# Kernel tuning notes

Hardware: AMD Instinct MI355X
Metric: run time of the kernel (lower is better)

Reference implementation:

```python
import jax, jax.numpy as jnp
import numpy as np

BLOCK = 256


def setup_inputs() -> dict:
    key = jax.random.key(0)
    ks = jax.random.split(key, 6)
    b, n, hid = 2, 4096, 2048
    h, d = 16, 128
    x = jax.random.normal(ks[0], (b, n, hid), dtype=jnp.float32)
    slope_rate = jax.random.uniform(ks[1], (h, 1, 1), dtype=jnp.float32)
    Wqkv = jax.random.normal(ks[2], (3 * h * d, hid), dtype=jnp.float32) * 0.02
    Wg = jax.random.normal(ks[3], (h * d, hid), dtype=jnp.float32) * 0.02
    norm_w = jnp.ones((h * d,), dtype=jnp.float32)
    Wo = jax.random.normal(ks[4], (hid, h * d), dtype=jnp.float32) * 0.02
    return {"x": x, "slope_rate": slope_rate, "Wqkv": Wqkv, "Wg": Wg, "norm_w": norm_w, "Wo": Wo}


def reference(x, slope_rate, Wqkv, Wg, norm_w, Wo):
    b, n, hid = x.shape
    h = slope_rate.shape[0]
    d = Wqkv.shape[0] // (3 * h)
    nb = n // BLOCK

    qkv = jax.nn.silu(x @ Wqkv.T).reshape(b, n, h, 3 * d)
    q, k, v = jnp.split(qkv, 3, axis=-1)           # each (b, n, h, d)
    # -> (b, h, n, d)
    q = q.transpose(0, 2, 1, 3)
    k = k.transpose(0, 2, 1, 3)
    v = v.transpose(0, 2, 1, 3)

    s = slope_rate.astype(jnp.float32)             # (h, 1, 1)
    arr = jnp.arange(1, BLOCK + 1, dtype=jnp.float32)
    q_decay = jnp.exp(-s * arr[:, None])           # (h, BLOCK, 1)
    k_decay = jnp.exp(-s * (BLOCK - arr[:, None])) # (h, BLOCK, 1)
    idx = arr[:, None] - arr[None, :]              # (BLOCK, BLOCK)
    diag_decay = jnp.where(idx >= 0, jnp.exp(-s * idx), 0.0)  # (h, BLOCK, BLOCK)
    block_decay = jnp.exp(-s * BLOCK)              # (h, 1, 1)

    # chunk into blocks: (nb, b, h, BLOCK, d)
    def chunk(t):
        return t.reshape(b, h, nb, BLOCK, d).transpose(2, 0, 1, 3, 4)
    qc, kc, vc = chunk(q), chunk(k), chunk(v)

    def step(kv, qkv_blk):
        qi, ki, vi = qkv_blk
        # inter-block: decayed query against running kv state
        out_nd = jnp.einsum('bhmd,bhde->bhme', qi * q_decay, kv)
        # intra-block: decay-masked quadratic attention
        qk = jnp.einsum('bhmd,bhnd->bhmn', qi, ki) * diag_decay
        out_d = jnp.einsum('bhmn,bhne->bhme', qk, vi)
        kv_new = block_decay * kv + jnp.einsum('bhmd,bhme->bhde', ki * k_decay, vi)
        return kv_new, out_nd + out_d

    kv0 = jnp.zeros((b, h, d, d), dtype=jnp.float32)
    _, out_blocks = jax.lax.scan(step, kv0, (qc, kc, vc))  # (nb, b, h, BLOCK, d)

    out = out_blocks.transpose(1, 2, 0, 3, 4).reshape(b, h, n, d)
    out = out.transpose(0, 2, 1, 3).reshape(b, n, h * d)  # b n (h d)

    # RMSNorm
    eps = jnp.finfo(jnp.float32).eps
    rms = jax.lax.rsqrt(jnp.mean(out * out, axis=-1, keepdims=True) + eps)
    out = out * rms * norm_w

    gate = jax.nn.sigmoid(x @ Wg.T)
    return (gate * out) @ Wo.T
```

## Files before the change

### kernel.cpp

```cpp
#include <hip/hip_runtime.h>
#include <stdint.h>

typedef __attribute__((ext_vector_type(8))) short short8;
typedef __attribute__((ext_vector_type(4))) float f32x4;

#define DEV static __device__ __forceinline__

DEV float b2f(unsigned short u) {
  unsigned x = ((unsigned)u) << 16;
  return __builtin_bit_cast(float, x);
}
DEV unsigned short f2b(float f) {
  unsigned x = __builtin_bit_cast(unsigned, f);
  return (unsigned short)((x + 0x7fffu + ((x >> 16) & 1u)) >> 16);
}
DEV void gload16(const unsigned short* g, unsigned short* l) {
  __builtin_amdgcn_global_load_lds((const __attribute__((address_space(1))) void*)g,
                                   (__attribute__((address_space(3))) void*)l, 16, 0, 0);
}
#define MFMA(a, b, c) __builtin_amdgcn_mfma_f32_16x16x32_bf16(a, b, c, 0, 0, 0)

__global__ void k_f2b(const float* __restrict__ in, unsigned short* __restrict__ out, long n) {
  long i = ((long)blockIdx.x * blockDim.x + threadIdx.x) * 4;
  long stride = (long)gridDim.x * blockDim.x * 4;
  for (; i < n; i += stride) {
    float4 f = *(const float4*)(in + i);
    ushort4 o;
    o.x = f2b(f.x); o.y = f2b(f.y); o.z = f2b(f.z); o.w = f2b(f.w);
    *(ushort4*)(out + i) = o;
  }
}

template <int MODE>
__global__ __launch_bounds__(256, 2) void k_gemm(
    const unsigned short* __restrict__ A, const unsigned short* __restrict__ B0,
    const unsigned short* __restrict__ B1, int K, int NB0,
    unsigned short* __restrict__ o_q, unsigned short* __restrict__ o_k,
    unsigned short* __restrict__ o_v, unsigned short* __restrict__ o_g,
    float* __restrict__ o_f) {
  __shared__ unsigned short a_sh[128 * 32];
  __shared__ unsigned short b_sh[128 * 32];
  int tid = threadIdx.x;
  int w = tid >> 6, lane = tid & 63;
  int brow = blockIdx.x * 128, bcol = blockIdx.y * 128;
  const unsigned short* Bt = (MODE == 1 || bcol < NB0) ? (B0 + (size_t)bcol * K)
                                                       : (B1 + (size_t)(bcol - NB0) * K);
  int wrow = (w >> 1) * 64, wcol = (w & 1) * 64;
  f32x4 acc[4][4];
#pragma unroll
  for (int m = 0; m < 4; m++)
#pragma unroll
    for (int n = 0; n < 4; n++) acc[m][n] = (f32x4)0.f;

  int srow = lane >> 2;
  int scol = (lane & 3) * 8;
  int nk = K >> 5;
  for (int it = 0; it < nk; ++it) {
    int kt = it << 5;
    __syncthreads();
#pragma unroll
    for (int c = 0; c < 2; ++c) {
      int hseg = w * 2 + c;
      int row = hseg * 16 + srow;
      gload16(A + (size_t)(brow + row) * K + kt + scol, a_sh + hseg * 512 + lane * 8);
      gload16(Bt + (size_t)row * K + kt + scol, b_sh + hseg * 512 + lane * 8);
    }
    __syncthreads();
    int ko = (lane >> 4) * 8;
    short8 af[4], bfr[4];
#pragma unroll
    for (int m = 0; m < 4; m++)
      af[m] = *(const short8*)(a_sh + (wrow + m * 16 + (lane & 15)) * 32 + ko);
#pragma unroll
    for (int n = 0; n < 4; n++)
      bfr[n] = *(const short8*)(b_sh + (wcol + n * 16 + (lane & 15)) * 32 + ko);
#pragma unroll
    for (int m = 0; m < 4; m++)
#pragma unroll
      for (int n = 0; n < 4; n++) acc[m][n] = MFMA(af[m], bfr[n], acc[m][n]);
  }
#pragma unroll
  for (int m = 0; m < 4; m++) {
#pragma unroll
    for (int r = 0; r < 4; r++) {
      int row = brow + wrow + m * 16 + (lane >> 4) * 4 + r;
#pragma unroll
      for (int n = 0; n < 4; n++) {
        int col = bcol + wcol + n * 16 + (lane & 15);
        float v = acc[m][n][r];
        if (MODE == 0) {
          if (col < 6144) {
            float sv = v / (1.f + __expf(-v));
            int h = col / 384, dd = col - h * 384;
            int b = row >> 12, t = row & 4095;
            size_t base = ((size_t)(b * 16 + h) * 4096 + t) * 128;
            if (dd < 128) o_q[base + dd] = f2b(sv);
            else if (dd < 256) o_k[base + dd - 128] = f2b(sv);
            else o_v[base + dd - 256] = f2b(sv);
          } else {
            float gv = 1.f / (1.f + __expf(-v));
            o_g[(size_t)row * 2048 + (col - 6144)] = f2b(gv);
          }
        } else {
          o_f[(size_t)row * ((size_t)gridDim.y * 128) + col] = v;
        }
      }
    }
  }
}

__global__ __launch_bounds__(256) void k_kvblk(const unsigned short* __restrict__ kk,
                                               const unsigned short* __restrict__ vv,
                                               const float* __restrict__ slope,
                                               unsigned short* __restrict__ kvT) {
  int gid = blockIdx.x;
  int bh = gid >> 4, blk = gid & 15;
  float s = slope[bh & 15];
  __shared__ unsigned short kT[128][72];
  __shared__ unsigned short vT[128][72];
  int tid = threadIdx.x, w = tid >> 6, lane = tid & 63;
  int wrow = (w >> 1) * 64, wcol = (w & 1) * 64;
  f32x4 acc[4][4];
#pragma unroll
  for (int m = 0; m < 4; m++)
#pragma unroll
    for (int n = 0; n < 4; n++) acc[m][n] = (f32x4)0.f;
  const unsigned short* kb = kk + ((size_t)bh * 4096 + blk * 256) * 128;
  const unsigned short* vb = vv + ((size_t)bh * 4096 + blk * 256) * 128;
  int tt = tid & 63, c0 = (tid >> 6) * 32;
  for (int tc = 0; tc < 4; ++tc) {
    __syncthreads();
    int tg = tc * 64 + tt;
    float kd = __expf(-s * (float)(255 - tg));
#pragma unroll
    for (int g = 0; g < 4; ++g) {
      int c = c0 + g * 8;
      short8 k8 = *(const short8*)(kb + (size_t)tg * 128 + c);
      short8 v8 = *(const short8*)(vb + (size_t)tg * 128 + c);
#pragma unroll
      for (int j = 0; j < 8; ++j) {
        kT[c + j][tt] = f2b(b2f((unsigned short)k8[j]) * kd);
        vT[c + j][tt] = (unsigned short)v8[j];
      }
    }
    __syncthreads();
#pragma unroll
    for (int kx = 0; kx < 64; kx += 32) {
      int ko = kx + (lane >> 4) * 8;
      short8 af[4], bfr[4];
#pragma unroll
      for (int m = 0; m < 4; m++) af[m] = *(const short8*)&vT[wrow + m * 16 + (lane & 15)][ko];
#pragma unroll
      for (int n = 0; n < 4; n++) bfr[n] = *(const short8*)&kT[wcol + n * 16 + (lane & 15)][ko];
#pragma unroll
      for (int m = 0; m < 4; m++)
#pragma unroll
        for (int n = 0; n < 4; n++) acc[m][n] = MFMA(af[m], bfr[n], acc[m][n]);
    }
  }
  unsigned short* op = kvT + (size_t)gid * 16384;
#pragma unroll
  for (int m = 0; m < 4; m++)
#pragma unroll
    for (int r = 0; r < 4; r++) {
      int e = wrow + m * 16 + (lane >> 4) * 4 + r;
#pragma unroll
      for (int n = 0; n < 4; n++) {
        int d = wcol + n * 16 + (lane & 15);
        op[e * 128 + d] = f2b(acc[m][n][r]);
      }
    }
}

__global__ void k_scan(unsigned short* kvT, const float* __restrict__ slope) {
  int gid = blockIdx.x;
  int bh = gid >> 6;
  int eo = (gid & 63) * 256 + threadIdx.x;
  float s = slope[bh & 15];
  float bd = __expf(-s * 256.f);
  float st = 0.f;
  size_t base = (size_t)bh * 16 * 16384 + eo;
#pragma unroll
  for (int i = 0; i < 16; ++i) {
    unsigned short c = kvT[base + (size_t)i * 16384];
    kvT[base + (size_t)i * 16384] = f2b(st);
    st = bd * st + b2f(c);
  }
}

__global__ __launch_bounds__(256) void k_attn(const unsigned short* __restrict__ q,
                                              const unsigned short* __restrict__ kk,
                                              const unsigned short* __restrict__ vv,
                                              const unsigned short* __restrict__ kvT,
                                              const float* __restrict__ slope,
                                              unsigned short* __restrict__ attn) {
  int gid = blockIdx.x;
  int hf = gid & 1, blk = (gid >> 1) & 15, bh = gid >> 5;
  float s = slope[bh & 15];
  __shared__ unsigned short k_sh[64][136];
  __shared__ unsigned short vT_sh[128][72];
  __shared__ unsigned short s_sh[4][32][72];
  int tid = threadIdx.x, w = tid >> 6, lane = tid & 63;
  int mm0 = hf * 128 + w * 32;
  const unsigned short* qb = q + ((size_t)bh * 4096 + blk * 256) * 128;
  const unsigned short* kvb = kvT + (size_t)(bh * 16 + blk) * 16384;
  f32x4 acc[2][8];
#pragma unroll
  for (int m = 0; m < 2; m++)
#pragma unroll
    for (int n = 0; n < 8; n++) acc[m][n] = (f32x4)0.f;
#pragma unroll
  for (int kx = 0; kx < 128; kx += 32) {
    int ko = kx + (lane >> 4) * 8;
    short8 af[2], bfr[8];
#pragma unroll
    for (int mi = 0; mi < 2; mi++)
      af[mi] = *(const short8*)(qb + (size_t)(mm0 + mi * 16 + (lane & 15)) * 128 + ko);
#pragma unroll
    for (int ni = 0; ni < 8; ni++)
      bfr[ni] = *(const short8*)(kvb + (size_t)(ni * 16 + (lane & 15)) * 128 + ko);
#pragma unroll
    for (int mi = 0; mi < 2; mi++)
#pragma unroll
      for (int ni = 0; ni < 8; ni++) acc[mi][ni] = MFMA(af[mi], bfr[ni], acc[mi][ni]);
  }
#pragma unroll
  for (int mi = 0; mi < 2; mi++)
#pragma unroll
    for (int r = 0; r < 4; r++) {
      float qd = __expf(-s * (float)(mm0 + mi * 16 + (lane >> 4) * 4 + r + 1));
#pragma unroll
      for (int ni = 0; ni < 8; ni++) acc[mi][ni][r] *= qd;
    }
  int nchunk = 2 * (hf + 1);
  for (int tc = 0; tc < nchunk; ++tc) {
    __syncthreads();
    {
      int t2 = tid >> 2, c = (tid & 3) * 32;
      const unsigned short* kp = kk + ((size_t)bh * 4096 + blk * 256 + tc * 64 + t2) * 128 + c;
#pragma unroll
      for (int g = 0; g < 4; ++g) *(short8*)&k_sh[t2][c + g * 8] = *(const short8*)(kp + g * 8);
    }
    {
      int t2 = tid & 63, e0 = (tid >> 6) * 32;
      const unsigned short* vp = vv + ((size_t)bh * 4096 + blk * 256 + tc * 64 + t2) * 128 + e0;
#pragma unroll
      for (int g = 0; g < 4; ++g) {
        short8 v8 = *(const short8*)(vp + g * 8);
#pragma unroll
        for (int j = 0; j < 8; ++j) vT_sh[e0 + g * 8 + j][t2] = (unsigned short)v8[j];
      }
    }
    __syncthreads();
    if (tc * 64 <= mm0 + 31) {
      f32x4 sa[2][4];
#pragma unroll
      for (int m = 0; m < 2; m++)
#pragma unroll
        for (int n = 0; n < 4; n++) sa[m][n] = (f32x4)0.f;
#pragma unroll
      for (int kx = 0; kx < 128; kx += 32) {
        int ko = kx + (lane >> 4) * 8;
        short8 af[2], bfr[4];
#pragma unroll
        for (int mi = 0; mi < 2; mi++)
          af[mi] = *(const short8*)(qb + (size_t)(mm0 + mi * 16 + (lane & 15)) * 128 + ko);
#pragma unroll
        for (int ni = 0; ni < 4; ni++) bfr[ni] = *(const short8*)&k_sh[ni * 16 + (lane & 15)][ko];
#pragma unroll
        for (int mi = 0; mi < 2; mi++)
#pragma unroll
          for (int ni = 0; ni < 4; ni++) sa[mi][ni] = MFMA(af[mi], bfr[ni], sa[mi][ni]);
      }
#pragma unroll
      for (int mi = 0; mi < 2; mi++)
#pragma unroll
        for (int ni = 0; ni < 4; ni++)
#pragma unroll
          for (int r = 0; r < 4; r++) {
            int mm = mm0 + mi * 16 + (lane >> 4) * 4 + r;
            int ttg = tc * 64 + ni * 16 + (lane & 15);
            int diff = mm - ttg;
            float val = (diff >= 0) ? sa[mi][ni][r] * __expf(-s * (float)diff) : 0.f;
            s_sh[w][mi * 16 + (lane >> 4) * 4 + r][ni * 16 + (lane & 15)] = f2b(val);
          }
#pragma unroll
      for (int k2 = 0; k2 < 64; k2 += 32) {
        int ko2 = k2 + (lane >> 4) * 8;
        short8 a2[2];
#pragma unroll
        for (int mi = 0; mi < 2; mi++)
          a2[mi] = *(const short8*)&s_sh[w][mi * 16 + (lane & 15)][ko2];
#pragma unroll
        for (int ni = 0; ni < 8; ni++) {
          short8 b2 = *(const short8*)&vT_sh[ni * 16 + (lane & 15)][ko2];
#pragma unroll
          for (int mi = 0; mi < 2; mi++) acc[mi][ni] = MFMA(a2[mi], b2, acc[mi][ni]);
        }
      }
    }
  }
  int b = bh >> 4, h = bh & 15;
#pragma unroll
  for (int mi = 0; mi < 2; mi++)
#pragma unroll
    for (int r = 0; r < 4; r++) {
      int mm = mm0 + mi * 16 + (lane >> 4) * 4 + r;
      size_t rowp = ((size_t)b * 4096 + blk * 256 + mm) * 2048 + h * 128;
#pragma unroll
      for (int ni = 0; ni < 8; ni++) attn[rowp + ni * 16 + (lane & 15)] = f2b(acc[mi][ni][r]);
    }
}

__global__ __launch_bounds__(256) void k_norm(const unsigned short* __restrict__ attn,
                                              const unsigned short* __restrict__ gate,
                                              const float* __restrict__ nw,
                                              unsigned short* __restrict__ y) {
  int row = blockIdx.x;
  int tid = threadIdx.x, w = tid >> 6, lane = tid & 63;
  const unsigned short* ap = attn + (size_t)row * 2048 + tid * 8;
  const unsigned short* gp = gate + (size_t)row * 2048 + tid * 8;
  short8 a8 = *(const short8*)ap;
  float vals[8];
  float ss = 0.f;
#pragma unroll
  for (int j = 0; j < 8; ++j) {
    vals[j] = b2f((unsigned short)a8[j]);
    ss += vals[j] * vals[j];
  }
#pragma unroll
  for (int off = 32; off > 0; off >>= 1) ss += __shfl_down(ss, off, 64);
  __shared__ float red[4];
  if (lane == 0) red[w] = ss;
  __syncthreads();
  float tot = red[0] + red[1] + red[2] + red[3];
  float rms = rsqrtf(tot * (1.f / 2048.f) + 1.1920929e-07f);
  short8 g8 = *(const short8*)gp;
  short8 o;
#pragma unroll
  for (int j = 0; j < 8; ++j)
    o[j] = (short)f2b(vals[j] * rms * nw[tid * 8 + j] * b2f((unsigned short)g8[j]));
  *(short8*)(y + (size_t)row * 2048 + tid * 8) = o;
}

extern "C" void kernel_launch(void* const* d_in, const int* in_sizes, int n_in, void* d_out,
                              int out_size, void* d_ws, size_t ws_size, hipStream_t stream) {
  const float* x = (const float*)d_in[0];
  const float* slope = (const float*)d_in[1];
  const float* Wqkv = (const float*)d_in[2];
  const float* Wg = (const float*)d_in[3];
  const float* nw = (const float*)d_in[4];
  const float* Wo = (const float*)d_in[5];
  float* out = (float*)d_out;

  unsigned short* q = (unsigned short*)d_ws;
  unsigned short* k = q + 16777216;
  unsigned short* v = k + 16777216;
  unsigned short* gate = v + 16777216;
  unsigned short* xb = gate + 16777216;
  unsigned short* wqkvb = xb + 16777216;
  unsigned short* wgb = wqkvb + 12582912;
  unsigned short* wob = wgb + 4194304;
  unsigned short* kvT = wob + 4194304;
  unsigned short* attn = wqkvb;
  unsigned short* y = xb;

  k_f2b<<<2048, 256, 0, stream>>>(x, xb, 16777216L);
  k_f2b<<<2048, 256, 0, stream>>>(Wqkv, wqkvb, 12582912L);
  k_f2b<<<1024, 256, 0, stream>>>(Wg, wgb, 4194304L);
  k_f2b<<<1024, 256, 0, stream>>>(Wo, wob, 4194304L);

  k_gemm<0><<<dim3(64, 64), 256, 0, stream>>>(xb, wqkvb, wgb, 2048, 6144, q, k, v, gate, nullptr);
  k_kvblk<<<512, 256, 0, stream>>>(k, v, slope, kvT);
  k_scan<<<2048, 256, 0, stream>>>(kvT, slope);
  k_attn<<<1024, 256, 0, stream>>>(q, k, v, kvT, slope, attn);
  k_norm<<<8192, 256, 0, stream>>>(attn, gate, nw, y);
  k_gemm<1><<<dim3(64, 16), 256, 0, stream>>>(y, wob, nullptr, 2048, 1 << 30, nullptr, nullptr,
                                              nullptr, nullptr, out);
}
```

Baseline: 547.4 us.

## Rewrite GEMM with 256x256 tiles, 8 waves, double-buffered swizzled LDS pipeline

Replaces the 128x128, 4-wave, single-stage GEMM with a 256x256 tile using 8 waves. K steps of 64 are double-buffered in 128KB of LDS and loaded asynchronously with global_load_lds, using explicit vmcnt waits and barriers. LDS columns are XOR-swizzled to avoid bank conflicts, block IDs are remapped for L2 locality, and s_setprio is raised around the MFMA phases. The goal is to overlap global loads with compute and raise arithmetic intensity. In exchange it uses far more LDS and registers, hardcodes K=2048 and the 6144 split, and with 128KB of LDS per block it likely fits only one block per CU despite the launch bound of 2.

```diff
diff --git a/kernel.cpp b/kernel.cpp
--- a/kernel.cpp
+++ b/kernel.cpp
@@ -32,62 +32,109 @@
 }
 
 template <int MODE>
-__global__ __launch_bounds__(256, 2) void k_gemm(
+__global__ __launch_bounds__(512, 2) void k_gemm(
     const unsigned short* __restrict__ A, const unsigned short* __restrict__ B0,
-    const unsigned short* __restrict__ B1, int K, int NB0,
+    const unsigned short* __restrict__ B1,
     unsigned short* __restrict__ o_q, unsigned short* __restrict__ o_k,
     unsigned short* __restrict__ o_v, unsigned short* __restrict__ o_g,
     float* __restrict__ o_f) {
-  __shared__ unsigned short a_sh[128 * 32];
-  __shared__ unsigned short b_sh[128 * 32];
-  int tid = threadIdx.x;
-  int w = tid >> 6, lane = tid & 63;
-  int brow = blockIdx.x * 128, bcol = blockIdx.y * 128;
-  const unsigned short* Bt = (MODE == 1 || bcol < NB0) ? (B0 + (size_t)bcol * K)
-                                                       : (B1 + (size_t)(bcol - NB0) * K);
-  int wrow = (w >> 1) * 64, wcol = (w & 1) * 64;
-  f32x4 acc[4][4];
-#pragma unroll
-  for (int m = 0; m < 4; m++)
+  const int K = 2048, NT = 32;
+  __shared__ unsigned short sm[65536];
+  int tid = threadIdx.x, w = tid >> 6, lane = tid & 63;
+  int wm = w >> 2, wn = w & 3;
+  int l15 = lane & 15, l4 = lane >> 4;
+  int cpx = gridDim.x >> 3;
+  int bid = blockIdx.x;
+  int swz = (bid & 7) * cpx + (bid >> 3);
+  int tm = swz & 31, tn = swz >> 5;
+  int brow = tm << 8, bcol = tn << 8;
+  const unsigned short* Ab = A + (size_t)brow * K;
+  const unsigned short* Bb = (MODE == 1 || bcol < 6144) ? (B0 + (size_t)bcol * K)
+                                                        : (B1 + (size_t)(bcol - 6144) * K);
+  f32x4 acc[8][4];
+#pragma unroll
+  for (int m = 0; m < 8; m++)
 #pragma unroll
     for (int n = 0; n < 4; n++) acc[m][n] = (f32x4)0.f;
 
-  int srow = lane >> 2;
-  int scol = (lane & 3) * 8;
-  int nk = K >> 5;
-  for (int it = 0; it < nk; ++it) {
-    int kt = it << 5;
-    __syncthreads();
-#pragma unroll
-    for (int c = 0; c < 2; ++c) {
-      int hseg = w * 2 + c;
-      int row = hseg * 16 + srow;
-      gload16(A + (size_t)(brow + row) * K + kt + scol, a_sh + hseg * 512 + lane * 8);
-      gload16(Bt + (size_t)row * K + kt + scol, b_sh + hseg * 512 + lane * 8);
-    }
-    __syncthreads();
-    int ko = (lane >> 4) * 8;
-    short8 af[4], bfr[4];
-#pragma unroll
-    for (int m = 0; m < 4; m++)
-      af[m] = *(const short8*)(a_sh + (wrow + m * 16 + (lane & 15)) * 32 + ko);
-#pragma unroll
-    for (int n = 0; n < 4; n++)
-      bfr[n] = *(const short8*)(b_sh + (wcol + n * 16 + (lane & 15)) * 32 + ko);
-#pragma unroll
-    for (int m = 0; m < 4; m++)
-#pragma unroll
-      for (int n = 0; n < 4; n++) acc[m][n] = MFMA(af[m], bfr[n], acc[m][n]);
-  }
-#pragma unroll
-  for (int m = 0; m < 4; m++) {
-#pragma unroll
-    for (int r = 0; r < 4; r++) {
-      int row = brow + wrow + m * 16 + (lane >> 4) * 4 + r;
-#pragma unroll
-      for (int n = 0; n < 4; n++) {
-        int col = bcol + wcol + n * 16 + (lane & 15);
-        float v = acc[m][n][r];
+  auto stage = [&](int U) {
+    if (U >= 4 * NT) return;
+    int tt = U >> 2, s = U & 3;
+    unsigned short* lb = sm + (tt & 1) * 32768 + s * 8192;
+    int kt = tt << 6;
+#pragma unroll
+    for (int i = 0; i < 2; ++i) {
+      int c = i * 512 + tid;
+      int pos = c >> 3, pb = c & 7;
+      int gcol = kt + ((pb ^ (pos & 7)) << 3);
+      const unsigned short* src;
+      if (s == 0) src = Ab + (size_t)((pos >> 6) * 128 + (pos & 63)) * K + gcol;
+      else if (s == 2) src = Ab + (size_t)((pos >> 6) * 128 + 64 + (pos & 63)) * K + gcol;
+      else if (s == 1) src = Bb + (size_t)((pos >> 5) * 64 + (pos & 31)) * K + gcol;
+      else src = Bb + (size_t)((pos >> 5) * 64 + 32 + (pos & 31)) * K + gcol;
+      gload16(src, lb + c * 8);
+    }
+  };
+
+  for (int U = 0; U < 6; ++U) stage(U);
+  asm volatile("s_waitcnt vmcnt(8)" ::: "memory");
+  __builtin_amdgcn_s_barrier();
+  asm volatile("" ::: "memory");
+
+  for (int T = 0; T < NT; ++T) {
+    const unsigned short* bufb = sm + (T & 1) * 32768;
+#pragma unroll
+    for (int p = 0; p < 4; ++p) {
+      const int mh = p >> 1, nh = p & 1;
+      const unsigned short* Abase = bufb + (mh ? 2 : 0) * 8192;
+      const unsigned short* Bbase = bufb + (nh ? 3 : 1) * 8192;
+      short8 af[4][2], bfr[2][2];
+#pragma unroll
+      for (int mi = 0; mi < 4; ++mi) {
+        int pos = wm * 64 + mi * 16 + l15;
+        int px = pos * 64, hh = pos & 7;
+#pragma unroll
+        for (int ks = 0; ks < 2; ++ks)
+          af[mi][ks] = *(const short8*)(Abase + px + (((ks * 4 + l4) ^ hh) << 3));
+      }
+#pragma unroll
+      for (int ni = 0; ni < 2; ++ni) {
+        int pos = wn * 32 + ni * 16 + l15;
+        int px = pos * 64, hh = pos & 7;
+#pragma unroll
+        for (int ks = 0; ks < 2; ++ks)
+          bfr[ni][ks] = *(const short8*)(Bbase + px + (((ks * 4 + l4) ^ hh) << 3));
+      }
+      stage(4 * T + p + 6);
+      asm volatile("" ::: "memory");
+      __builtin_amdgcn_s_barrier();
+      asm volatile("" ::: "memory");
+      __builtin_amdgcn_s_setprio(1);
+#pragma unroll
+      for (int mi = 0; mi < 4; ++mi)
+#pragma unroll
+        for (int ni = 0; ni < 2; ++ni)
+#pragma unroll
+          for (int ks = 0; ks < 2; ++ks)
+            acc[mh * 4 + mi][nh * 2 + ni] =
+                MFMA(af[mi][ks], bfr[ni][ks], acc[mh * 4 + mi][nh * 2 + ni]);
+      __builtin_amdgcn_s_setprio(0);
+      if (p == 0 || p == 2) asm volatile("s_waitcnt vmcnt(6)" ::: "memory");
+      asm volatile("" ::: "memory");
+      __builtin_amdgcn_s_barrier();
+      asm volatile("" ::: "memory");
+    }
+  }
+
+#pragma unroll
+  for (int mi = 0; mi < 8; ++mi)
+#pragma unroll
+    for (int r = 0; r < 4; ++r) {
+      int row = brow + wm * 128 + mi * 16 + l4 * 4 + r;
+#pragma unroll
+      for (int ni = 0; ni < 4; ++ni) {
+        int col = bcol + wn * 64 + ni * 16 + l15;
+        float v = acc[mi][ni][r];
         if (MODE == 0) {
           if (col < 6144) {
             float sv = v / (1.f + __expf(-v));
@@ -102,11 +149,10 @@
             o_g[(size_t)row * 2048 + (col - 6144)] = f2b(gv);
           }
         } else {
-          o_f[(size_t)row * ((size_t)gridDim.y * 128) + col] = v;
+          o_f[(size_t)row * 2048 + col] = v;
         }
       }
     }
-  }
 }
 
 __global__ __launch_bounds__(256) void k_kvblk(const unsigned short* __restrict__ kk,
@@ -370,11 +416,10 @@
   k_f2b<<<1024, 256, 0, stream>>>(Wg, wgb, 4194304L);
   k_f2b<<<1024, 256, 0, stream>>>(Wo, wob, 4194304L);
 
-  k_gemm<0><<<dim3(64, 64), 256, 0, stream>>>(xb, wqkvb, wgb, 2048, 6144, q, k, v, gate, nullptr);
+  k_gemm<0><<<1024, 512, 0, stream>>>(xb, wqkvb, wgb, q, k, v, gate, nullptr);
   k_kvblk<<<512, 256, 0, stream>>>(k, v, slope, kvT);
   k_scan<<<2048, 256, 0, stream>>>(kvT, slope);
   k_attn<<<1024, 256, 0, stream>>>(q, k, v, kvT, slope, attn);
   k_norm<<<8192, 256, 0, stream>>>(attn, gate, nw, y);
-  k_gemm<1><<<dim3(64, 16), 256, 0, stream>>>(y, wob, nullptr, 2048, 1 << 30, nullptr, nullptr,
-                                              nullptr, nullptr, out);
-}
+  k_gemm<1><<<256, 512, 0, stream>>>(y, wob, nullptr, nullptr, nullptr, nullptr, nullptr, out);
+}
```

After: 568.5 us. +3.8%, slower.
